# Optimization experiments

Hardware: AMD Instinct MI355X
Metric: run time of the kernel (lower is better)

The kernel has to match this reference:

```python
import jax, jax.numpy as jnp
import numpy as np

BETA = 0.25

def setup_inputs() -> dict:
    key = jax.random.key(0)
    kz, ke = jax.random.split(key)
    z = jax.random.normal(kz, (8, 256, 8, 32, 32), dtype=jnp.float32)
    num_codes, code_dim = 1024, 256
    # matches nn.init.uniform_(weight, -1/num_codes, 1/num_codes) in scale
    embed = jax.random.uniform(ke, (num_codes, code_dim), dtype=jnp.float32,
                               minval=-1.0 / num_codes, maxval=1.0 / num_codes)
    return {"z": z, "embed": embed}


def reference(z, embed):
    # z: (B, C, D, H, W); embed: (num_codes, code_dim) with C == code_dim
    B, C, D, H, W = z.shape
    num_codes = embed.shape[0]
    z_flat = jnp.transpose(z, (0, 2, 3, 4, 1)).reshape(-1, C)  # (N, C)

    # squared euclidean distances to all codes: ||z||^2 + ||e||^2 - 2 z.e
    dist = ((z_flat * z_flat).sum(axis=1, keepdims=True)
            + (embed * embed).sum(axis=1)
            - 2.0 * z_flat @ embed.T)  # (N, num_codes)
    indices = jnp.argmin(dist, axis=1)  # (N,) int
    z_q_flat = embed[indices]  # (N, C) gather

    # commitment loss (codebook is EMA-updated, so only beta * commitment)
    commitment = jnp.mean((z_flat - jax.lax.stop_gradient(z_q_flat)) ** 2)
    loss = BETA * commitment

    # straight-through estimator
    z_q_flat = z_flat + jax.lax.stop_gradient(z_q_flat - z_flat)
    z_q = jnp.transpose(z_q_flat.reshape(B, D, H, W, C), (0, 4, 1, 2, 3))

    # perplexity (scatter-add histogram instead of materializing one-hot)
    counts = jnp.zeros((num_codes,), dtype=z.dtype).at[indices].add(1.0)
    avg_probs = counts / indices.shape[0]
    perplexity = jnp.exp(-jnp.sum(avg_probs * jnp.log(avg_probs + 1e-10)))

    return z_q, indices.reshape(B, D, H, W), loss, perplexity
```

## Files before the change

### kernel.cpp

```cpp
#include <hip/hip_runtime.h>
#include <math.h>

#define Cdim   256
#define Ssp    8192
#define Npts   65536
#define NCODES 1024
#define BETA   0.25f
#define MT     128
#define NKC    48
#define ESCALE 8192.0f
#define WS_NEED (65536 + (size_t)786432 * 2)

typedef _Float16 f16;
typedef f16   half8  __attribute__((ext_vector_type(8)));
typedef float f32x16 __attribute__((ext_vector_type(16)));

#define MFMA16(A, B, C) __builtin_amdgcn_mfma_f32_32x32x16_f16(A, B, C, 0, 0, 0)

__global__ __launch_bounds__(256) void enorm_kernel(const float* __restrict__ embed,
                                                    float* __restrict__ enorm) {
    int j = blockIdx.x * 256 + threadIdx.x;
    if (j >= NCODES) return;
    const float4* row = reinterpret_cast<const float4*>(embed + (size_t)j * Cdim);
    float s = 0.f;
#pragma unroll 8
    for (int c4 = 0; c4 < Cdim / 4; ++c4) {
        float4 v = row[c4];
        s += v.x * v.x + v.y * v.y + v.z * v.z + v.w * v.w;
    }
    enorm[j] = s;
}

__global__ __launch_bounds__(256) void prep_kernel(const float* __restrict__ embed,
                                                   f16* __restrict__ Bws) {
    int tid = blockIdx.x * 256 + threadIdx.x;
    int o4 = tid * 4;
    int kc = o4 >> 14;
    int r  = o4 & 16383;
    int j  = r >> 4;
    int k0 = r & 15;
#pragma unroll
    for (int i = 0; i < 4; ++i) {
        int k = kc * 16 + k0 + i;
        int c = k & 255;
        float ev = embed[j * 256 + c] * ESCALE;
        f16 eh = (f16)ev;
        f16 v  = (k >= 256 && k < 512) ? (f16)(ev - (float)eh) : eh;
        Bws[o4 + i] = v;
    }
}

#define GG(k) (((k) < 16) ? (2 * (k) + kb) : ((k) < 32) ? (2 * ((k) - 16) + kb) \
                                                        : (32 + 2 * ((k) - 32) + kb))

__global__ __launch_bounds__(512, 2) void vq_gemm(const float* __restrict__ z,
                                                  const f16* __restrict__ Bws,
                                                  const float* __restrict__ enorm,
                                                  float* __restrict__ out_idx,
                                                  float* __restrict__ loss_acc,
                                                  float* __restrict__ counts) {
    __shared__ __attribute__((aligned(16))) f16 As[MT * 512];
    __shared__ float en_s[NCODES];
    __shared__ float znp[4 * MT];
    __shared__ float zn_s[MT];
    __shared__ float redv[8 * MT];
    __shared__ int   redi[8 * MT];

    const int t  = threadIdx.x;
    const int l  = t & 63;
    const int w  = t >> 6;
    const int wm = w >> 2;
    const int wn = w & 3;
    const int ln = l & 31;
    const int kb = l >> 5;
    const int n0 = blockIdx.x * MT;
    const int b  = n0 >> 13;
    const int s0 = n0 & 8191;

    {
        const int p = t & 127;
        const int q = t >> 7;
        const float* zb = z + (size_t)b * ((size_t)Cdim * Ssp) + s0;
        float zsq = 0.f;
#pragma unroll
        for (int gi = 0; gi < 8; ++gi) {
            const int c0 = q * 64 + gi * 8;
            half8 hh, ll;
#pragma unroll
            for (int u = 0; u < 8; ++u) {
                float zv = zb[(size_t)(c0 + u) * Ssp + p];
                zsq += zv * zv;
                f16 zh = (f16)zv;
                hh[u] = zh;
                ll[u] = (f16)(zv - (float)zh);
            }
            const int g0 = c0 >> 3;
            *(half8*)&As[p * 512 + 8 * (g0 ^ (p & 7))]        = hh;
            *(half8*)&As[p * 512 + 8 * ((32 + g0) ^ (p & 7))] = ll;
        }
        znp[q * MT + p] = zsq;
    }
    for (int i = t; i < NCODES; i += 512) en_s[i] = enorm[i];
    __syncthreads();
    if (t < MT)
        zn_s[t] = ((znp[t] + znp[MT + t]) + znp[2 * MT + t]) + znp[3 * MT + t];
    __syncthreads();

    const int rowA = wm * 64 + ln;

#define LOADG(kcv, A0, A1, B0, B1, B2, B3)                               \
    {                                                                    \
        const int ggx  = GG(kcv);                                        \
        const int gswx = 8 * (ggx ^ (ln & 7));                           \
        A0 = *(const half8*)&As[rowA * 512 + gswx];                      \
        A1 = *(const half8*)&As[(rowA + 32) * 512 + gswx];               \
        const f16* srcx = bbase + (size_t)(kcv) * 16384;                 \
        B0 = *(const half8*)(srcx);                                      \
        B1 = *(const half8*)(srcx + 512);                                \
        B2 = *(const half8*)(srcx + 1024);                               \
        B3 = *(const half8*)(srcx + 1536);                               \
    }

#define MFMAG(A0, A1, B0, B1, B2, B3)                                    \
    __builtin_amdgcn_s_setprio(1);                                       \
    acc[0][0] = MFMA16(A0, B0, acc[0][0]);                               \
    acc[1][0] = MFMA16(A1, B0, acc[1][0]);                               \
    acc[0][1] = MFMA16(A0, B1, acc[0][1]);                               \
    acc[1][1] = MFMA16(A1, B1, acc[1][1]);                               \
    acc[0][2] = MFMA16(A0, B2, acc[0][2]);                               \
    acc[1][2] = MFMA16(A1, B2, acc[1][2]);                               \
    acc[0][3] = MFMA16(A0, B3, acc[0][3]);                               \
    acc[1][3] = MFMA16(A1, B3, acc[1][3]);                               \
    __builtin_amdgcn_s_setprio(0);

#pragma unroll 1
    for (int jh = 0; jh < 2; ++jh) {
        f32x16 acc[2][4] = {};
        const f16* bbase = Bws + (size_t)(jh * 512 + wn * 128 + ln) * 16 + kb * 8;

        half8 aA0, aA1, bA0, bA1, bA2, bA3;
        half8 aB0, aB1, bB0, bB1, bB2, bB3;
        LOADG(0, aA0, aA1, bA0, bA1, bA2, bA3)

#pragma unroll 1
        for (int kc = 0; kc < NKC; kc += 2) {
            LOADG(kc + 1, aB0, aB1, bB0, bB1, bB2, bB3)
            __builtin_amdgcn_sched_barrier(0);
            MFMAG(aA0, aA1, bA0, bA1, bA2, bA3)
            __builtin_amdgcn_sched_barrier(0);

            const int kc2 = (kc + 2 < NKC) ? kc + 2 : NKC - 1;
            LOADG(kc2, aA0, aA1, bA0, bA1, bA2, bA3)
            __builtin_amdgcn_sched_barrier(0);
            MFMAG(aB0, aB1, bB0, bB1, bB2, bB3)
            __builtin_amdgcn_sched_barrier(0);
        }

        const int h = l >> 5;
#pragma unroll
        for (int mm = 0; mm < 2; ++mm) {
#pragma unroll
            for (int rg = 0; rg < 16; ++rg) {
                const int row = wm * 64 + mm * 32 + (rg & 3) + 8 * (rg >> 2) + 4 * h;
                const float znv = zn_s[row];
                float bv = 3.0e38f; int bi = 0;
#pragma unroll
                for (int nn = 0; nn < 4; ++nn) {
                    const int col = jh * 512 + wn * 128 + nn * 32 + ln;
                    float k1 = znv + en_s[col];
                    float sc = k1 - acc[mm][nn][rg] * (2.0f / ESCALE);
                    if (sc < bv) { bv = sc; bi = col; }
                }
#pragma unroll
                for (int off = 1; off < 32; off <<= 1) {
                    float ov = __shfl_xor(bv, off, 64);
                    int   oi = __shfl_xor(bi, off, 64);
                    if (ov < bv || (ov == bv && oi < bi)) { bv = ov; bi = oi; }
                }
                if (ln == 0) {
                    redv[(jh * 4 + wn) * MT + row] = bv;
                    redi[(jh * 4 + wn) * MT + row] = bi;
                }
            }
        }
    }
    __syncthreads();

    if (t < MT) {
        float bv = redv[t]; int bi = redi[t];
#pragma unroll
        for (int s = 1; s < 8; ++s) {
            float ov = redv[s * MT + t]; int oi = redi[s * MT + t];
            if (ov < bv || (ov == bv && oi < bi)) { bv = ov; bi = oi; }
        }
        out_idx[n0 + t] = (float)bi;
        atomicAdd(&counts[bi], 1.0f);
        float lsum = bv;
#pragma unroll
        for (int off = 32; off > 0; off >>= 1) lsum += __shfl_down(lsum, off, 64);
        if ((t & 63) == 0) atomicAdd(loss_acc, lsum);
    }
#undef LOADG
#undef MFMAG
}

__global__ __launch_bounds__(256) void vq_epi(const float* __restrict__ embed,
                                              const float* __restrict__ out_idx,
                                              float* __restrict__ out_zq) {
    const int n = blockIdx.x * 256 + threadIdx.x;
    const int b = n >> 13, s = n & 8191;
    const int idx = (int)out_idx[n];
    const float4* er = reinterpret_cast<const float4*>(embed + (size_t)idx * Cdim);
    float* oq = out_zq + (size_t)b * ((size_t)Cdim * Ssp) + s;
#pragma unroll 4
    for (int c4 = 0; c4 < Cdim / 4; ++c4) {
        float4 e = er[c4];
        const int c = c4 * 4;
        __builtin_nontemporal_store(e.x, oq + (size_t)(c + 0) * Ssp);
        __builtin_nontemporal_store(e.y, oq + (size_t)(c + 1) * Ssp);
        __builtin_nontemporal_store(e.z, oq + (size_t)(c + 2) * Ssp);
        __builtin_nontemporal_store(e.w, oq + (size_t)(c + 3) * Ssp);
    }
}

#define PTS 64
#define CT  128
#define KC  32
__global__ __launch_bounds__(256, 2) void vq_main_fb(const float* __restrict__ z,
                                                     const float* __restrict__ embed,
                                                     const float* __restrict__ enorm,
                                                     float* __restrict__ out_zq,
                                                     float* __restrict__ out_idx,
                                                     float* __restrict__ loss_acc,
                                                     float* __restrict__ counts) {
    __shared__ __attribute__((aligned(16))) float smem[Cdim * PTS + KC * CT];
    float* zt = smem;
    float* et = smem + Cdim * PTS;
    const int t  = threadIdx.x;
    const int n0 = blockIdx.x * PTS;
    const int b  = n0 >> 13;
    const int s0 = n0 & 8191;
    const float* zb = z + (size_t)b * Cdim * Ssp + s0;
    {
        const int p4 = (t & 15) * 4, crow = t >> 4;
#pragma unroll
        for (int it = 0; it < 16; ++it) {
            int c = it * 16 + crow;
            float4 v = *reinterpret_cast<const float4*>(zb + (size_t)c * Ssp + p4);
            *reinterpret_cast<float4*>(&zt[c * PTS + p4]) = v;
        }
    }
    __syncthreads();
    {
        const int p = t & 63, qq = t >> 6;
        float sacc = 0.f;
#pragma unroll 8
        for (int c = qq * 64; c < qq * 64 + 64; ++c) { float v = zt[c * PTS + p]; sacc += v * v; }
        et[qq * 64 + p] = sacc;
    }
    __syncthreads();
    const int pg = t & 15, jg = t >> 4;
    const int p0 = pg * 4;
    float zn[4];
#pragma unroll
    for (int i = 0; i < 4; ++i) {
        int p = p0 + i;
        zn[i] = ((et[p] + et[64 + p]) + et[128 + p]) + et[192 + p];
    }
    float bestv[4] = {3.0e38f, 3.0e38f, 3.0e38f, 3.0e38f};
    int   besti[4] = {0, 0, 0, 0};
    const int dj = t >> 3, q = t & 7;
    const int sw_st = (q & 3) << 3;
    for (int jt = 0; jt < NCODES / CT; ++jt) {
        const int J0 = jt * CT;
        float acc[4][8];
#pragma unroll
        for (int i = 0; i < 4; ++i)
#pragma unroll
            for (int m = 0; m < 8; ++m) acc[i][m] = 0.f;
        for (int ks = 0; ks < Cdim / KC; ++ks) {
            const int cc0 = ks * KC;
            __syncthreads();
#pragma unroll
            for (int i = 0; i < 4; ++i) {
                const int jrel = dj + 32 * i;
                const float4 v = *reinterpret_cast<const float4*>(
                    embed + (size_t)(J0 + jrel) * Cdim + cc0 + q * 4);
                const int c0 = q * 4;
                const int jsw = jrel ^ sw_st;
                et[(c0 + 0) * CT + jsw] = v.x;
                et[(c0 + 1) * CT + jsw] = v.y;
                et[(c0 + 2) * CT + jsw] = v.z;
                et[(c0 + 3) * CT + jsw] = v.w;
            }
            __syncthreads();
#pragma unroll 4
            for (int c = 0; c < KC; ++c) {
                const float4 zp = *reinterpret_cast<const float4*>(&zt[(cc0 + c) * PTS + p0]);
                const int jb = (jg * 8) ^ (((c >> 2) & 3) << 3);
                const float4 ea = *reinterpret_cast<const float4*>(&et[c * CT + jb]);
                const float4 eb = *reinterpret_cast<const float4*>(&et[c * CT + jb + 4]);
                const float zc[4] = {zp.x, zp.y, zp.z, zp.w};
                const float ec[8] = {ea.x, ea.y, ea.z, ea.w, eb.x, eb.y, eb.z, eb.w};
#pragma unroll
                for (int i = 0; i < 4; ++i)
#pragma unroll
                    for (int m = 0; m < 8; ++m) acc[i][m] += zc[i] * ec[m];
            }
        }
#pragma unroll
        for (int m = 0; m < 8; ++m) {
            const int cid = J0 + jg * 8 + m;
            const float en = enorm[cid];
#pragma unroll
            for (int i = 0; i < 4; ++i) {
                float k1 = zn[i] + en;
                float sc = k1 - 2.0f * acc[i][m];
                if (sc < bestv[i]) { bestv[i] = sc; besti[i] = cid; }
            }
        }
    }
    __syncthreads();
    float* rv = et; int* ri = (int*)(et + 1024); int* idxf = (int*)(et + 2048);
#pragma unroll
    for (int i = 0; i < 4; ++i) { int p = p0 + i; rv[p * 16 + jg] = bestv[i]; ri[p * 16 + jg] = besti[i]; }
    __syncthreads();
    if (t < PTS) {
        int p = t;
        float bv = rv[p * 16]; int bi = ri[p * 16];
        for (int g = 1; g < 16; ++g) {
            float v = rv[p * 16 + g]; int ii = ri[p * 16 + g];
            if (v < bv || (v == bv && ii < bi)) { bv = v; bi = ii; }
        }
        idxf[p] = bi;
        out_idx[n0 + p] = (float)bi;
        atomicAdd(&counts[bi], 1.0f);
    }
    __syncthreads();
    float lsum = 0.f;
    {
        const int p = t & 63, cbase = t >> 6;
        const int myidx = idxf[p];
        const float4* erow4 = reinterpret_cast<const float4*>(embed + (size_t)myidx * Cdim);
        float* ob = out_zq + (size_t)b * Cdim * Ssp + s0 + p;
#pragma unroll 4
        for (int pass = 0; pass < 16; ++pass) {
            int c = cbase * 64 + pass * 4;
            float4 e = erow4[c >> 2];
            ob[(size_t)(c + 0) * Ssp] = e.x;
            ob[(size_t)(c + 1) * Ssp] = e.y;
            ob[(size_t)(c + 2) * Ssp] = e.z;
            ob[(size_t)(c + 3) * Ssp] = e.w;
            float d0 = zt[(c + 0) * PTS + p] - e.x;
            float d1 = zt[(c + 1) * PTS + p] - e.y;
            float d2 = zt[(c + 2) * PTS + p] - e.z;
            float d3 = zt[(c + 3) * PTS + p] - e.w;
            lsum += d0 * d0 + d1 * d1 + d2 * d2 + d3 * d3;
        }
    }
#pragma unroll
    for (int off = 32; off > 0; off >>= 1) lsum += __shfl_down(lsum, off, 64);
    if ((t & 63) == 0) atomicAdd(loss_acc, lsum);
}

__global__ __launch_bounds__(1024) void vq_final(const float* __restrict__ counts,
                                                 const float* __restrict__ loss_acc,
                                                 float* __restrict__ out_loss,
                                                 float* __restrict__ out_perp) {
    __shared__ float red[16];
    int t = threadIdx.x;
    float cnt = counts[t];
    float avg = cnt * (1.0f / (float)Npts);
    float term = avg * logf(avg + 1e-10f);
#pragma unroll
    for (int off = 32; off > 0; off >>= 1) term += __shfl_down(term, off, 64);
    if ((t & 63) == 0) red[t >> 6] = term;
    __syncthreads();
    if (t == 0) {
        float s = 0.f;
        for (int i = 0; i < 16; ++i) s += red[i];
        *out_perp = expf(-s);
        *out_loss = BETA * loss_acc[0] * (1.0f / 16777216.0f);
    }
}

extern "C" void kernel_launch(void* const* d_in, const int* in_sizes, int n_in,
                              void* d_out, int out_size, void* d_ws, size_t ws_size,
                              hipStream_t stream) {
    const float* z     = (const float*)d_in[0];
    const float* embed = (const float*)d_in[1];

    float* ws       = (float*)d_ws;
    float* loss_acc = ws;
    float* counts   = ws + 64;
    float* enorm    = ws + 2048;

    float* out_zq   = (float*)d_out;
    float* out_idx  = out_zq + (size_t)Npts * Cdim;
    float* out_loss = out_idx + Npts;
    float* out_perp = out_loss + 1;

    hipMemsetAsync(d_ws, 0, 2048 * sizeof(float), stream);
    enorm_kernel<<<NCODES / 256, 256, 0, stream>>>(embed, enorm);

    if (ws_size >= WS_NEED) {
        f16* Bws = (f16*)((char*)d_ws + 65536);
        prep_kernel<<<768, 256, 0, stream>>>(embed, Bws);
        vq_gemm<<<Npts / MT, 512, 0, stream>>>(z, Bws, enorm, out_idx,
                                               loss_acc, counts);
        vq_epi<<<Npts / 256, 256, 0, stream>>>(embed, out_idx, out_zq);
    } else {
        vq_main_fb<<<Npts / PTS, 256, 0, stream>>>(z, embed, enorm, out_zq, out_idx,
                                                   loss_acc, counts);
    }
    vq_final<<<1, 1024, 0, stream>>>(counts, loss_acc, out_loss, out_perp);
}
```

Baseline: 200.7 us.

## Reuse high-half codebook fragments for both z hi and lo MFMA passes

The split-precision GEMM previously walked 48 k-chunks, each loading its own B fragment, even though the z-hi and z-lo passes multiply the same e-hi data. The loop is now split in two. The first phase loads e-hi once per chunk and issues MFMAs against both the z-hi and z-lo A fragments. The second phase handles z-hi times e-lo. This cuts global/L2 B traffic by a third and shrinks the prepared codebook buffer to 32 chunks, so prep launches fewer blocks. The cost is higher register pressure from holding extra A fragments in flight, which could hurt occupancy or cause spills.

New measurement: 197.7 us. About the same (-1.5%).

```diff
diff --git a/kernel.cpp b/kernel.cpp
--- a/kernel.cpp
+++ b/kernel.cpp
@@ -7,7 +7,6 @@
 #define NCODES 1024
 #define BETA   0.25f
 #define MT     128
-#define NKC    48
 #define ESCALE 8192.0f
 #define WS_NEED (65536 + (size_t)786432 * 2)
 
@@ -45,13 +44,10 @@
         int c = k & 255;
         float ev = embed[j * 256 + c] * ESCALE;
         f16 eh = (f16)ev;
-        f16 v  = (k >= 256 && k < 512) ? (f16)(ev - (float)eh) : eh;
+        f16 v  = (k >= 256) ? (f16)(ev - (float)eh) : eh;
         Bws[o4 + i] = v;
     }
 }
-
-#define GG(k) (((k) < 16) ? (2 * (k) + kb) : ((k) < 32) ? (2 * ((k) - 16) + kb) \
-                                                        : (32 + 2 * ((k) - 32) + kb))
 
 __global__ __launch_bounds__(512, 2) void vq_gemm(const float* __restrict__ z,
                                                   const f16* __restrict__ Bws,
@@ -108,20 +104,58 @@
 
     const int rowA = wm * 64 + ln;
 
-#define LOADG(kcv, A0, A1, B0, B1, B2, B3)                               \
+#define LOADGE(kcv, H0, H1, L0, L1, B0, B1, B2, B3)                      \
     {                                                                    \
-        const int ggx  = GG(kcv);                                        \
-        const int gswx = 8 * (ggx ^ (ln & 7));                           \
-        A0 = *(const half8*)&As[rowA * 512 + gswx];                      \
-        A1 = *(const half8*)&As[(rowA + 32) * 512 + gswx];               \
-        const f16* srcx = bbase + (size_t)(kcv) * 16384;                 \
+        const int kcl_ = ((kcv) < 16) ? (kcv) : 15;                      \
+        const int gz   = 2 * kcl_ + kb;                                  \
+        const int gwh  = 8 * (gz ^ (ln & 7));                            \
+        const int gwl  = 8 * ((32 + gz) ^ (ln & 7));                     \
+        H0 = *(const half8*)&As[rowA * 512 + gwh];                       \
+        H1 = *(const half8*)&As[(rowA + 32) * 512 + gwh];                \
+        L0 = *(const half8*)&As[rowA * 512 + gwl];                       \
+        L1 = *(const half8*)&As[(rowA + 32) * 512 + gwl];                \
+        const f16* srcx = bbase + (size_t)kcl_ * 16384;                  \
         B0 = *(const half8*)(srcx);                                      \
         B1 = *(const half8*)(srcx + 512);                                \
         B2 = *(const half8*)(srcx + 1024);                               \
         B3 = *(const half8*)(srcx + 1536);                               \
     }
 
-#define MFMAG(A0, A1, B0, B1, B2, B3)                                    \
+#define MFMAGE(H0, H1, L0, L1, B0, B1, B2, B3)                           \
+    __builtin_amdgcn_s_setprio(1);                                       \
+    acc[0][0] = MFMA16(H0, B0, acc[0][0]);                               \
+    acc[1][0] = MFMA16(H1, B0, acc[1][0]);                               \
+    acc[0][1] = MFMA16(H0, B1, acc[0][1]);                               \
+    acc[1][1] = MFMA16(H1, B1, acc[1][1]);                               \
+    acc[0][2] = MFMA16(H0, B2, acc[0][2]);                               \
+    acc[1][2] = MFMA16(H1, B2, acc[1][2]);                               \
+    acc[0][3] = MFMA16(H0, B3, acc[0][3]);                               \
+    acc[1][3] = MFMA16(H1, B3, acc[1][3]);                               \
+    acc[0][0] = MFMA16(L0, B0, acc[0][0]);                               \
+    acc[1][0] = MFMA16(L1, B0, acc[1][0]);                               \
+    acc[0][1] = MFMA16(L0, B1, acc[0][1]);                               \
+    acc[1][1] = MFMA16(L1, B1, acc[1][1]);                               \
+    acc[0][2] = MFMA16(L0, B2, acc[0][2]);                               \
+    acc[1][2] = MFMA16(L1, B2, acc[1][2]);                               \
+    acc[0][3] = MFMA16(L0, B3, acc[0][3]);                               \
+    acc[1][3] = MFMA16(L1, B3, acc[1][3]);                               \
+    __builtin_amdgcn_s_setprio(0);
+
+#define LOADGL(kcv, A0, A1, B0, B1, B2, B3)                              \
+    {                                                                    \
+        const int kcl_ = ((kcv) < 32) ? (kcv) : 31;                      \
+        const int gz   = 2 * (kcl_ - 16) + kb;                           \
+        const int gwh  = 8 * (gz ^ (ln & 7));                            \
+        A0 = *(const half8*)&As[rowA * 512 + gwh];                       \
+        A1 = *(const half8*)&As[(rowA + 32) * 512 + gwh];                \
+        const f16* srcx = bbase + (size_t)kcl_ * 16384;                  \
+        B0 = *(const half8*)(srcx);                                      \
+        B1 = *(const half8*)(srcx + 512);                                \
+        B2 = *(const half8*)(srcx + 1024);                               \
+        B3 = *(const half8*)(srcx + 1536);                               \
+    }
+
+#define MFMAGL(A0, A1, B0, B1, B2, B3)                                   \
     __builtin_amdgcn_s_setprio(1);                                       \
     acc[0][0] = MFMA16(A0, B0, acc[0][0]);                               \
     acc[1][0] = MFMA16(A1, B0, acc[1][0]);                               \
@@ -133,27 +167,44 @@
     acc[1][3] = MFMA16(A1, B3, acc[1][3]);                               \
     __builtin_amdgcn_s_setprio(0);
 
+#define SB __builtin_amdgcn_sched_barrier(0);
+
 #pragma unroll 1
     for (int jh = 0; jh < 2; ++jh) {
         f32x16 acc[2][4] = {};
         const f16* bbase = Bws + (size_t)(jh * 512 + wn * 128 + ln) * 16 + kb * 8;
 
-        half8 aA0, aA1, bA0, bA1, bA2, bA3;
-        half8 aB0, aB1, bB0, bB1, bB2, bB3;
-        LOADG(0, aA0, aA1, bA0, bA1, bA2, bA3)
-
+        {
+            half8 hA0, hA1, lA0, lA1, bA0, bA1, bA2, bA3;
+            half8 hB0, hB1, lB0, lB1, bB0, bB1, bB2, bB3;
+            LOADGE(0, hA0, hA1, lA0, lA1, bA0, bA1, bA2, bA3)
 #pragma unroll 1
-        for (int kc = 0; kc < NKC; kc += 2) {
-            LOADG(kc + 1, aB0, aB1, bB0, bB1, bB2, bB3)
-            __builtin_amdgcn_sched_barrier(0);
-            MFMAG(aA0, aA1, bA0, bA1, bA2, bA3)
-            __builtin_amdgcn_sched_barrier(0);
-
-            const int kc2 = (kc + 2 < NKC) ? kc + 2 : NKC - 1;
-            LOADG(kc2, aA0, aA1, bA0, bA1, bA2, bA3)
-            __builtin_amdgcn_sched_barrier(0);
-            MFMAG(aB0, aB1, bB0, bB1, bB2, bB3)
-            __builtin_amdgcn_sched_barrier(0);
+            for (int kc = 0; kc < 16; kc += 2) {
+                LOADGE(kc + 1, hB0, hB1, lB0, lB1, bB0, bB1, bB2, bB3)
+                SB
+                MFMAGE(hA0, hA1, lA0, lA1, bA0, bA1, bA2, bA3)
+                SB
+                LOADGE(kc + 2, hA0, hA1, lA0, lA1, bA0, bA1, bA2, bA3)
+                SB
+                MFMAGE(hB0, hB1, lB0, lB1, bB0, bB1, bB2, bB3)
+                SB
+            }
+        }
+        {
+            half8 aA0, aA1, bA0, bA1, bA2, bA3;
+            half8 aB0, aB1, bB0, bB1, bB2, bB3;
+            LOADGL(16, aA0, aA1, bA0, bA1, bA2, bA3)
+#pragma unroll 1
+            for (int kc = 16; kc < 32; kc += 2) {
+                LOADGL(kc + 1, aB0, aB1, bB0, bB1, bB2, bB3)
+                SB
+                MFMAGL(aA0, aA1, bA0, bA1, bA2, bA3)
+                SB
+                LOADGL(kc + 2, aA0, aA1, bA0, bA1, bA2, bA3)
+                SB
+                MFMAGL(aB0, aB1, bB0, bB1, bB2, bB3)
+                SB
+            }
         }
 
         const int h = l >> 5;
@@ -200,8 +251,11 @@
         for (int off = 32; off > 0; off >>= 1) lsum += __shfl_down(lsum, off, 64);
         if ((t & 63) == 0) atomicAdd(loss_acc, lsum);
     }
-#undef LOADG
-#undef MFMAG
+#undef LOADGE
+#undef MFMAGE
+#undef LOADGL
+#undef MFMAGL
+#undef SB
 }
 
 __global__ __launch_bounds__(256) void vq_epi(const float* __restrict__ embed,
@@ -405,7 +459,7 @@
 
     if (ws_size >= WS_NEED) {
         f16* Bws = (f16*)((char*)d_ws + 65536);
-        prep_kernel<<<768, 256, 0, stream>>>(embed, Bws);
+        prep_kernel<<<512, 256, 0, stream>>>(embed, Bws);
         vq_gemm<<<Npts / MT, 512, 0, stream>>>(z, Bws, enorm, out_idx,
                                                loss_acc, counts);
         vq_epi<<<Npts / 256, 256, 0, stream>>>(embed, out_idx, out_zq);
```
